# Kernel optimization log

Measured on AMD Instinct MI355X. Metric: run time of the kernel, lower is better.

Reference implementation:

```python
import jax, jax.numpy as jnp
import numpy as np

N_GRAPHS = 256      # graphs in the batch
N_PER = 52          # nodes per peptide graph (module default num_nodes=52)
IN_CH = 21          # amino-acid one-hot features
HIDDEN = 128
OUT_EG = 128
LATENT = 64
N_LAYERS = 4


def _fc_edges(n_graphs, n_per):
    """Block-diagonal fully-connected directed edges (no self loops)."""
    base = np.arange(n_per)
    r, c = np.meshgrid(base, base, indexing='ij')
    mask = r != c
    r, c = r[mask], c[mask]                       # [n_per*(n_per-1)]
    offs = (np.arange(n_graphs) * n_per)[:, None]
    row = (r[None, :] + offs).reshape(-1)
    col = (c[None, :] + offs).reshape(-1)
    return row.astype(np.int32), col.astype(np.int32)


def setup_inputs() -> dict:
    key = jax.random.key(0)
    ks = iter(jax.random.split(key, 40))

    def rn(shape, scale=0.05):
        return jax.random.normal(next(ks), shape, dtype=jnp.float32) * scale

    N = N_GRAPHS * N_PER
    row, col = _fc_edges(N_GRAPHS, N_PER)
    L, H = N_LAYERS, HIDDEN
    return {
        'x': jax.random.normal(next(ks), (N, IN_CH), dtype=jnp.float32),
        'pos': jax.random.normal(next(ks), (N, 3), dtype=jnp.float32),
        'edge_row': jnp.asarray(row),
        'edge_col': jnp.asarray(col),
        'batch': jnp.repeat(jnp.arange(N_GRAPHS, dtype=jnp.int32), N_PER),
        'emb_in_w': rn((IN_CH, H)), 'emb_in_b': jnp.zeros((H,), jnp.float32),
        'edge_w1': rn((L, 2 * H + 1, H)), 'edge_b1': jnp.zeros((L, H), jnp.float32),
        'edge_w2': rn((L, H, H)), 'edge_b2': jnp.zeros((L, H), jnp.float32),
        'node_w1': rn((L, 2 * H, H)), 'node_b1': jnp.zeros((L, H), jnp.float32),
        'node_w2': rn((L, H, H)), 'node_b2': jnp.zeros((L, H), jnp.float32),
        'coord_w1': rn((L, H, H)), 'coord_b1': jnp.zeros((L, H), jnp.float32),
        'coord_w2': rn((L, H, 1), scale=0.001),   # xavier gain=0.001, no bias
        'emb_out_w': rn((H, OUT_EG)), 'emb_out_b': jnp.zeros((OUT_EG,), jnp.float32),
        'mean_w': rn((OUT_EG, LATENT)), 'mean_b': jnp.zeros((LATENT,), jnp.float32),
        'logvar_w': rn((OUT_EG, LATENT)), 'logvar_b': jnp.zeros((LATENT,), jnp.float32),
    }


def _segment_mean(data, ids, n):
    s = jax.ops.segment_sum(data, ids, num_segments=n)
    cnt = jax.ops.segment_sum(jnp.ones((data.shape[0],), data.dtype), ids, num_segments=n)
    return s / jnp.clip(cnt, 1.0)[:, None]


def _egcl(h, coord, row, col, p):
    """One E_GCL layer (residual=True, coords_agg='mean', no attention/tanh/normalize)."""
    ew1, eb1, ew2, eb2, nw1, nb1, nw2, nb2, cw1, cb1, cw2 = p
    n = h.shape[0]
    coord_diff = coord[row] - coord[col]                     # [E,3]
    radial = jnp.sum(coord_diff * coord_diff, axis=1, keepdims=True)  # [E,1]
    # edge model
    m = jnp.concatenate([h[row], h[col], radial], axis=1)    # [E,2H+1]
    m = jax.nn.silu(m @ ew1 + eb1)
    edge_feat = jax.nn.silu(m @ ew2 + eb2)                   # [E,H]
    # coord model: per-edge scalar, mean-aggregated onto source nodes
    t = jax.nn.silu(edge_feat @ cw1 + cb1) @ cw2             # [E,1]
    coord = coord + _segment_mean(coord_diff * t, row, n)
    # node model: sum-aggregate edge features, MLP, residual
    agg = jax.ops.segment_sum(edge_feat, row, num_segments=n)
    z = jnp.concatenate([h, agg], axis=1)                    # [N,2H]
    z = jax.nn.silu(z @ nw1 + nb1)
    h = h + (z @ nw2 + nb2)
    return h, coord


def reference(x, pos, edge_row, edge_col, batch,
              emb_in_w, emb_in_b,
              edge_w1, edge_b1, edge_w2, edge_b2,
              node_w1, node_b1, node_w2, node_b2,
              coord_w1, coord_b1, coord_w2,
              emb_out_w, emb_out_b,
              mean_w, mean_b, logvar_w, logvar_b):
    h = x @ emb_in_w + emb_in_b
    coord = pos
    for i in range(edge_w1.shape[0]):
        h, coord = _egcl(h, coord, edge_row, edge_col,
                         (edge_w1[i], edge_b1[i], edge_w2[i], edge_b2[i],
                          node_w1[i], node_b1[i], node_w2[i], node_b2[i],
                          coord_w1[i], coord_b1[i], coord_w2[i]))
    h = h @ emb_out_w + emb_out_b                            # embedding_out
    g = _segment_mean(h, batch, N_GRAPHS)                    # global_mean_pool
    mean = g @ mean_w + mean_b
    log_var = g @ logvar_w + logvar_b
    return mean, log_var
```

## Files before the change

### kernel.cpp

```cpp
#include <hip/hip_runtime.h>

constexpr int NPER = 52;
constexpr int HID  = 128;
constexpr int INCH = 21;
constexpr int NLAY = 4;
constexpr int LATD = 64;
constexpr int NGRAPH = 256;
constexpr int TPB  = 1024;
constexpr int TSTR = 424;
constexpr int TILE = 16 * TSTR;

typedef short short8 __attribute__((ext_vector_type(8)));
typedef float f32x4  __attribute__((ext_vector_type(4)));

constexpr int W1T_OFF = 0;
constexpr int W1T_SZ  = NLAY * 256 * HID;
constexpr int W2T_OFF = W1T_OFF + W1T_SZ;
constexpr int W2T_SZ  = NLAY * HID * HID;
constexpr int C1T_OFF = W2T_OFF + W2T_SZ;
constexpr int C1T_SZ  = NLAY * HID * HID;
constexpr int N1T_OFF = C1T_OFF + C1T_SZ;
constexpr int N1T_SZ  = NLAY * HID * 2 * HID;
constexpr int N2T_OFF = N1T_OFF + N1T_SZ;
constexpr int N2T_SZ  = NLAY * HID * HID;
constexpr int WS_ELEMS = N2T_OFF + N2T_SZ;

__device__ __forceinline__ unsigned cvt_pk_bf16(float a, float b) {
    unsigned r;
    asm("v_cvt_pk_bf16_f32 %0, %1, %2" : "=v"(r) : "v"(a), "v"(b));
    return r;
}
__device__ __forceinline__ unsigned short f2bf(float f) {
    return (unsigned short)cvt_pk_bf16(f, f);
}
__device__ __forceinline__ float bf2f(unsigned short h) {
    return __uint_as_float(((unsigned)h) << 16);
}
__device__ __forceinline__ float fast_rcp(float x) {
    float r;
    asm("v_rcp_f32 %0, %1" : "=v"(r) : "v"(x));
    return r;
}
__device__ __forceinline__ float silu_f(float v) {
    return v * fast_rcp(1.0f + __expf(-v));
}
__device__ __forceinline__ f32x4 mfma16(short8 a, short8 b, f32x4 c) {
    return __builtin_amdgcn_mfma_f32_16x16x32_bf16(a, b, c, 0, 0, 0);
}

__device__ __forceinline__ int tidx(int row, int e) {
    return (e >> 3) * TSTR + row * 8 + (e & 7);
}

__global__ void conv_w(const float* __restrict__ ew1, const float* __restrict__ ew2,
                       const float* __restrict__ cw1, const float* __restrict__ nw1,
                       const float* __restrict__ nw2, unsigned short* __restrict__ ws)
{
    int idx = blockIdx.x * 256 + threadIdx.x;
    if (idx >= WS_ELEMS) return;
    float v;
    if (idx < W2T_OFF) {
        int t = idx - W1T_OFF;
        int L = t / (256 * HID), rem = t % (256 * HID);
        int n = rem / HID, k = rem % HID;
        v = (n < HID) ? ew1[(size_t)L * 257 * HID + k * HID + n]
                      : ew1[(size_t)L * 257 * HID + (HID + k) * HID + (n - HID)];
    } else if (idx < C1T_OFF) {
        int t = idx - W2T_OFF;
        int L = t / (HID * HID), rem = t % (HID * HID);
        int n = rem / HID, k = rem % HID;
        v = ew2[(size_t)L * HID * HID + k * HID + n];
    } else if (idx < N1T_OFF) {
        int t = idx - C1T_OFF;
        int L = t / (HID * HID), rem = t % (HID * HID);
        int n = rem / HID, k = rem % HID;
        v = cw1[(size_t)L * HID * HID + k * HID + n];
    } else if (idx < N2T_OFF) {
        int t = idx - N1T_OFF;
        int L = t / (HID * 2 * HID), rem = t % (HID * 2 * HID);
        int n = rem / (2 * HID), k = rem % (2 * HID);
        v = nw1[(size_t)L * 2 * HID * HID + k * HID + n];
    } else {
        int t = idx - N2T_OFF;
        int L = t / (HID * HID), rem = t % (HID * HID);
        int n = rem / HID, k = rem % HID;
        v = nw2[(size_t)L * HID * HID + k * HID + n];
    }
    ws[idx] = f2bf(v);
}

constexpr int LDS_FLOATS = 1024 + 156 + 156 + 128 + 512 + 128;
constexpr size_t SHMEM_BYTES = (size_t)8 * TILE * 2 + LDS_FLOATS * 4;

__device__ __forceinline__ void coord_agg(int r, int rr, const float* tpart,
                                          const float* coord_s, float* cacc_s, int lane)
{
    float dx = 0.f, dy = 0.f, dz = 0.f;
    if (lane < NPER) {
        const float* tb = tpart + rr * 256;
        float tc = tb[lane] + tb[64 + lane] + tb[128 + lane] + tb[192 + lane];
        dx = (coord_s[r * 3 + 0] - coord_s[lane * 3 + 0]) * tc;
        dy = (coord_s[r * 3 + 1] - coord_s[lane * 3 + 1]) * tc;
        dz = (coord_s[r * 3 + 2] - coord_s[lane * 3 + 2]) * tc;
    }
    #pragma unroll
    for (int m = 1; m < 64; m <<= 1) {
        dx += __shfl_xor(dx, m); dy += __shfl_xor(dy, m); dz += __shfl_xor(dz, m);
    }
    if (lane == 0) {
        cacc_s[r * 3 + 0] = dx; cacc_s[r * 3 + 1] = dy; cacc_s[r * 3 + 2] = dz;
    }
}

extern "C" __global__ void __launch_bounds__(TPB)
egnn_mfma(const float* __restrict__ x, const float* __restrict__ pos,
          const float* __restrict__ emb_in_w, const float* __restrict__ emb_in_b,
          const float* __restrict__ edge_w1,
          const float* __restrict__ edge_b1, const float* __restrict__ edge_b2,
          const float* __restrict__ node_b1, const float* __restrict__ node_b2,
          const float* __restrict__ coord_b1, const float* __restrict__ coord_w2,
          const float* __restrict__ emb_out_w, const float* __restrict__ emb_out_b,
          const float* __restrict__ mean_w, const float* __restrict__ mean_b,
          const float* __restrict__ logvar_w, const float* __restrict__ logvar_b,
          const unsigned short* __restrict__ ws, float* __restrict__ out)
{
    extern __shared__ __align__(16) char smem[];
    unsigned short* m0_t = (unsigned short*)smem;
    unsigned short* m1_t = m0_t + TILE;
    unsigned short* e0_t = m1_t + TILE;
    unsigned short* e1_t = e0_t + TILE;
    unsigned short* h_t  = e1_t + TILE;
    unsigned short* ag_t = h_t  + TILE;
    unsigned short* A_t  = ag_t + TILE;
    unsigned short* B_t  = A_t  + TILE;
    float* aggp    = (float*)(B_t + TILE);
    float* coord_s = aggp + 1024;
    float* cacc_s  = coord_s + 156;
    float* rad_s   = cacc_s + 156;
    float* tpart   = rad_s + 128;
    float* wr_s    = tpart + 512;

    const int g    = blockIdx.x;
    const int tid  = threadIdx.x;
    const int lane = tid & 63;
    const int wv   = tid >> 6;
    const int mp   = wv >> 2;
    const int np   = wv & 3;
    const int l15  = lane & 15;
    const int kb   = lane >> 4;
    const int rowA = mp * 16 + l15;
    const int crow0 = mp * 16 + kb * 4;
    const int n0   = 32 * np + l15;
    const int n1   = n0 + 16;
    const int jp   = 2 * lane;
    const int pb   = (jp >> 3) * TSTR + (jp & 7);
    const int fo   = kb * TSTR + rowA * 8;

    {
        float* xs = (float*)m0_t;
        for (int p = tid; p < NPER * INCH; p += TPB) xs[p] = x[(size_t)g * NPER * INCH + p];
        for (int p = tid; p < NPER * 3; p += TPB)    coord_s[p] = pos[(size_t)g * NPER * 3 + p];
    }
    __syncthreads();

    for (int p = tid; p < NPER * HID; p += TPB) {
        int c = p >> 7, j = p & 127;
        float s = emb_in_b[j];
        #pragma unroll 7
        for (int k = 0; k < INCH; ++k) s += ((float*)m0_t)[c * INCH + k] * emb_in_w[k * HID + j];
        h_t[tidx(c, j)] = f2bf(s);
    }
    __syncthreads();

    for (int L = 0; L < NLAY; ++L) {
        const unsigned short* w1t = ws + W1T_OFF + (size_t)L * 256 * HID;
        const unsigned short* w2t = ws + W2T_OFF + (size_t)L * HID * HID;
        const unsigned short* c1t = ws + C1T_OFF + (size_t)L * HID * HID;
        const unsigned short* n1t = ws + N1T_OFF + (size_t)L * HID * 2 * HID;
        const unsigned short* n2t = ws + N2T_OFF + (size_t)L * HID * HID;

        short8 wE[8], wC[8];
        #pragma unroll
        for (int s = 0; s < 4; ++s) {
            wE[s]     = *(const short8*)(w2t + (size_t)n0 * HID + 32 * s + 8 * kb);
            wE[4 + s] = *(const short8*)(w2t + (size_t)n1 * HID + 32 * s + 8 * kb);
            wC[s]     = *(const short8*)(c1t + (size_t)n0 * HID + 32 * s + 8 * kb);
            wC[4 + s] = *(const short8*)(c1t + (size_t)n1 * HID + 32 * s + 8 * kb);
        }
        float eb2v[2], cb1v[2], cw2v[2];
        eb2v[0] = edge_b2[L * HID + n0];  eb2v[1] = edge_b2[L * HID + n1];
        cb1v[0] = coord_b1[L * HID + n0]; cb1v[1] = coord_b1[L * HID + n1];
        cw2v[0] = coord_w2[L * HID + n0]; cw2v[1] = coord_w2[L * HID + n1];
        if (tid < HID) wr_s[tid] = edge_w1[(size_t)L * 257 * HID + 256 * HID + tid];

        {
            f32x4 acc[4];
            #pragma unroll
            for (int q = 0; q < 4; ++q) acc[q] = (f32x4){0.f, 0.f, 0.f, 0.f};
            #pragma unroll
            for (int s = 0; s < 4; ++s) {
                short8 af = *(const short8*)(h_t + fo + s * 4 * TSTR);
                #pragma unroll
                for (int q = 0; q < 4; ++q) {
                    int n = l15 + 16 * (4 * np + q);
                    short8 bf = *(const short8*)(w1t + (size_t)n * HID + 32 * s + 8 * kb);
                    acc[q] = mfma16(af, bf, acc[q]);
                }
            }
            #pragma unroll
            for (int q = 0; q < 4; ++q) {
                int n = l15 + 16 * (4 * np + q);
                float eb1 = (n < HID) ? edge_b1[L * HID + n] : 0.f;
                #pragma unroll
                for (int reg = 0; reg < 4; ++reg) {
                    int c = crow0 + reg;
                    if (c < NPER) {
                        float v = acc[q][reg] + eb1;
                        if (n < HID) A_t[tidx(c, n)] = f2bf(v);
                        else         B_t[tidx(c, n - HID)] = f2bf(v);
                    }
                }
            }
        }
        if (tid < NPER) {
            float dx = coord_s[0] - coord_s[tid * 3 + 0];
            float dy = coord_s[1] - coord_s[tid * 3 + 1];
            float dz = coord_s[2] - coord_s[tid * 3 + 2];
            rad_s[tid] = dx * dx + dy * dy + dz * dz;
        } else if (tid >= 64 && tid < 64 + NPER) {
            int c = tid - 64;
            float dx = coord_s[3] - coord_s[c * 3 + 0];
            float dy = coord_s[4] - coord_s[c * 3 + 1];
            float dz = coord_s[5] - coord_s[c * 3 + 2];
            rad_s[64 + c] = dx * dx + dy * dy + dz * dz;
        }
        __syncthreads();

        const float wrl = wr_s[jp], wrh = wr_s[jp + 1];

        for (int gp = 0; gp < 26; ++gp) {
            const int r0 = 2 * gp, r1 = r0 + 1;

            {
                unsigned pa0 = *(const unsigned*)(A_t + pb + r0 * 8);
                unsigned pa1 = *(const unsigned*)(A_t + pb + r1 * 8);
                float A0l = bf2f((unsigned short)(pa0 & 0xffff)), A0h = bf2f((unsigned short)(pa0 >> 16));
                float A1l = bf2f((unsigned short)(pa1 & 0xffff)), A1h = bf2f((unsigned short)(pa1 >> 16));
                for (int j = wv; j < 2 * NPER; j += 16) {
                    int rr = (j >= NPER);
                    int c  = rr ? j - NPER : j;
                    float Al = rr ? A1l : A0l, Ah = rr ? A1h : A0h;
                    float rad = rad_s[rr * 64 + c];
                    unsigned bp = *(const unsigned*)(B_t + pb + c * 8);
                    float v0 = Al + bf2f((unsigned short)(bp & 0xffff)) + rad * wrl;
                    float v1 = Ah + bf2f((unsigned short)(bp >> 16))    + rad * wrh;
                    unsigned mv = cvt_pk_bf16(silu_f(v0), silu_f(v1));
                    *(unsigned*)((rr ? m1_t : m0_t) + pb + c * 8) = mv;
                }
            }
            __syncthreads();

            {
                f32x4 e00 = (f32x4){0.f,0.f,0.f,0.f}, e01 = e00, e10 = e00, e11 = e00;
                #pragma unroll
                for (int s = 0; s < 4; ++s) {
                    short8 af0 = *(const short8*)(m0_t + fo + s * 4 * TSTR);
                    short8 af1 = *(const short8*)(m1_t + fo + s * 4 * TSTR);
                    e00 = mfma16(af0, wE[s], e00); e01 = mfma16(af0, wE[4 + s], e01);
                    e10 = mfma16(af1, wE[s], e10); e11 = mfma16(af1, wE[4 + s], e11);
                }
                #pragma unroll
                for (int rr = 0; rr < 2; ++rr) {
                    f32x4 ea = rr ? e10 : e00, eb = rr ? e11 : e01;
                    unsigned short* et = rr ? e1_t : e0_t;
                    const int r = rr ? r1 : r0;
                    float a0 = 0.f, a1 = 0.f;
                    #pragma unroll
                    for (int reg = 0; reg < 4; ++reg) {
                        int c = crow0 + reg;
                        float v0 = silu_f(ea[reg] + eb2v[0]);
                        float v1 = silu_f(eb[reg] + eb2v[1]);
                        if (c < NPER) {
                            et[tidx(c, n0)] = f2bf(v0);
                            et[tidx(c, n1)] = f2bf(v1);
                            if (c != r) { a0 += v0; a1 += v1; }
                        }
                    }
                    a0 += __shfl_xor(a0, 16); a0 += __shfl_xor(a0, 32);
                    a1 += __shfl_xor(a1, 16); a1 += __shfl_xor(a1, 32);
                    if (kb == 0) {
                        float* ar = aggp + (rr * 4 + mp) * HID;
                        ar[n0] = a0; ar[n1] = a1;
                    }
                }
                if (wv < 2 && gp > 0) coord_agg(2 * gp - 2 + wv, wv, tpart, coord_s, cacc_s, lane);
            }
            __syncthreads();

            {
                f32x4 y00 = (f32x4){0.f,0.f,0.f,0.f}, y01 = y00, y10 = y00, y11 = y00;
                #pragma unroll
                for (int s = 0; s < 4; ++s) {
                    short8 af0 = *(const short8*)(e0_t + fo + s * 4 * TSTR);
                    short8 af1 = *(const short8*)(e1_t + fo + s * 4 * TSTR);
                    y00 = mfma16(af0, wC[s], y00); y01 = mfma16(af0, wC[4 + s], y01);
                    y10 = mfma16(af1, wC[s], y10); y11 = mfma16(af1, wC[4 + s], y11);
                }
                #pragma unroll
                for (int rr = 0; rr < 2; ++rr) {
                    f32x4 ya = rr ? y10 : y00, yb = rr ? y11 : y01;
                    float* tp = tpart + (rr * 4 + np) * 64;
                    #pragma unroll
                    for (int reg = 0; reg < 4; ++reg) {
                        float v = silu_f(ya[reg] + cb1v[0]) * cw2v[0]
                                + silu_f(yb[reg] + cb1v[1]) * cw2v[1];
                        v += __shfl_xor(v, 1); v += __shfl_xor(v, 2);
                        v += __shfl_xor(v, 4); v += __shfl_xor(v, 8);
                        if (l15 == 0) tp[crow0 + reg] = v;
                    }
                }
            }
            if (tid < 256) {
                int rr = tid >> 7, t = tid & 127;
                const float* ap = aggp + rr * 512;
                float a = ap[t] + ap[128 + t] + ap[256 + t] + ap[384 + t];
                ag_t[tidx(2 * gp + rr, t)] = f2bf(a);
            } else if (tid < 384 && gp + 1 < 26) {
                int t = tid - 256, rr = t >> 6, c = t & 63;
                if (c < NPER) {
                    int r = 2 * (gp + 1) + rr;
                    float dx = coord_s[r * 3 + 0] - coord_s[c * 3 + 0];
                    float dy = coord_s[r * 3 + 1] - coord_s[c * 3 + 1];
                    float dz = coord_s[r * 3 + 2] - coord_s[c * 3 + 2];
                    rad_s[rr * 64 + c] = dx * dx + dy * dy + dz * dz;
                }
            }
            __syncthreads();
        }

        if (wv < 2) coord_agg(50 + wv, wv, tpart, coord_s, cacc_s, lane);
        {
            float nb1v[2];
            nb1v[0] = node_b1[L * HID + n0]; nb1v[1] = node_b1[L * HID + n1];
            f32x4 z0 = (f32x4){0.f,0.f,0.f,0.f}, z1 = z0;
            #pragma unroll
            for (int s = 0; s < 4; ++s) {
                short8 af = *(const short8*)(h_t + fo + s * 4 * TSTR);
                z0 = mfma16(af, *(const short8*)(n1t + (size_t)n0 * 2 * HID + 32 * s + 8 * kb), z0);
                z1 = mfma16(af, *(const short8*)(n1t + (size_t)n1 * 2 * HID + 32 * s + 8 * kb), z1);
            }
            #pragma unroll
            for (int s = 0; s < 4; ++s) {
                short8 af = *(const short8*)(ag_t + fo + s * 4 * TSTR);
                z0 = mfma16(af, *(const short8*)(n1t + (size_t)n0 * 2 * HID + HID + 32 * s + 8 * kb), z0);
                z1 = mfma16(af, *(const short8*)(n1t + (size_t)n1 * 2 * HID + HID + 32 * s + 8 * kb), z1);
            }
            #pragma unroll
            for (int reg = 0; reg < 4; ++reg) {
                int c = crow0 + reg;
                if (c < NPER) {
                    m0_t[tidx(c, n0)] = f2bf(silu_f(z0[reg] + nb1v[0]));
                    m0_t[tidx(c, n1)] = f2bf(silu_f(z1[reg] + nb1v[1]));
                }
            }
        }
        __syncthreads();

        if (tid < NPER * 3) coord_s[tid] += cacc_s[tid] * (1.0f / 51.0f);
        {
            float nb2v[2];
            nb2v[0] = node_b2[L * HID + n0]; nb2v[1] = node_b2[L * HID + n1];
            f32x4 d0 = (f32x4){0.f,0.f,0.f,0.f}, d1 = d0;
            #pragma unroll
            for (int s = 0; s < 4; ++s) {
                short8 af = *(const short8*)(m0_t + fo + s * 4 * TSTR);
                d0 = mfma16(af, *(const short8*)(n2t + (size_t)n0 * HID + 32 * s + 8 * kb), d0);
                d1 = mfma16(af, *(const short8*)(n2t + (size_t)n1 * HID + 32 * s + 8 * kb), d1);
            }
            #pragma unroll
            for (int reg = 0; reg < 4; ++reg) {
                int c = crow0 + reg;
                if (c < NPER) {
                    int i0 = tidx(c, n0), i1 = tidx(c, n1);
                    h_t[i0] = f2bf(bf2f(h_t[i0]) + d0[reg] + nb2v[0]);
                    h_t[i1] = f2bf(bf2f(h_t[i1]) + d1[reg] + nb2v[1]);
                }
            }
        }
        __syncthreads();
    }

    float* gm = aggp;
    float* eg = aggp + HID;
    if (tid < HID) {
        float s = 0.f;
        for (int c = 0; c < NPER; ++c) s += bf2f(h_t[tidx(c, tid)]);
        gm[tid] = s * (1.0f / 52.0f);
    }
    __syncthreads();
    if (tid < HID) {
        float s = emb_out_b[tid];
        #pragma unroll 4
        for (int k = 0; k < HID; ++k) s += gm[k] * emb_out_w[k * HID + tid];
        eg[tid] = s;
    }
    __syncthreads();
    if (tid < 2 * LATD) {
        const int  l   = tid & (LATD - 1);
        const bool ism = tid < LATD;
        const float* W = ism ? mean_w : logvar_w;
        float s = ism ? mean_b[l] : logvar_b[l];
        #pragma unroll 4
        for (int k = 0; k < HID; ++k) s += eg[k] * W[k * LATD + l];
        out[(ism ? 0 : NGRAPH * LATD) + g * LATD + l] = s;
    }
}

extern "C" void kernel_launch(void* const* d_in, const int* in_sizes, int n_in,
                              void* d_out, int out_size, void* d_ws, size_t ws_size,
                              hipStream_t stream) {
    const float* x         = (const float*)d_in[0];
    const float* pos       = (const float*)d_in[1];
    const float* emb_in_w  = (const float*)d_in[5];
    const float* emb_in_b  = (const float*)d_in[6];
    const float* edge_w1   = (const float*)d_in[7];
    const float* edge_b1   = (const float*)d_in[8];
    const float* edge_w2   = (const float*)d_in[9];
    const float* edge_b2   = (const float*)d_in[10];
    const float* node_w1   = (const float*)d_in[11];
    const float* node_b1   = (const float*)d_in[12];
    const float* node_w2   = (const float*)d_in[13];
    const float* node_b2   = (const float*)d_in[14];
    const float* coord_w1  = (const float*)d_in[15];
    const float* coord_b1  = (const float*)d_in[16];
    const float* coord_w2  = (const float*)d_in[17];
    const float* emb_out_w = (const float*)d_in[18];
    const float* emb_out_b = (const float*)d_in[19];
    const float* mean_w    = (const float*)d_in[20];
    const float* mean_b    = (const float*)d_in[21];
    const float* logvar_w  = (const float*)d_in[22];
    const float* logvar_b  = (const float*)d_in[23];

    unsigned short* ws = (unsigned short*)d_ws;

    conv_w<<<(WS_ELEMS + 255) / 256, 256, 0, stream>>>(edge_w1, edge_w2, coord_w1,
                                                       node_w1, node_w2, ws);

    (void)hipFuncSetAttribute(reinterpret_cast<const void*>(egnn_mfma),
                              hipFuncAttributeMaxDynamicSharedMemorySize,
                              (int)SHMEM_BYTES);

    hipLaunchKernelGGL(egnn_mfma, dim3(NGRAPH), dim3(TPB), SHMEM_BYTES, stream,
                       x, pos, emb_in_w, emb_in_b, edge_w1,
                       edge_b1, edge_b2, node_b1, node_b2,
                       coord_b1, coord_w2, emb_out_w, emb_out_b,
                       mean_w, mean_b, logvar_w, logvar_b,
                       ws, (float*)d_out);
}
```

Measured before the change: 805.7 us.

## Software-pipeline per-row edge stages into one barrier per phase

Replaces the two-rows-per-iteration loop, which had three barriers per row pair, with a 54-phase software pipeline. Each phase runs the edge-MLP MFMA for row r, the coord-MLP MFMA for row r-1, the message SiLU for row r+1, plus the aggregate reduction, radial and coordinate-update work on dedicated waves, all behind a single barrier. Weight fragments are now read from global/L2 inside the loop instead of being held in registers. The message step is vectorised to 4 elements per thread with the B operand hoisted, and SiLU uses raw exp/rcp instructions. This aims to cut barrier count and idle time, at the cost of repeated weight reloads and more pipeline logic.

```diff
diff --git a/kernel.cpp b/kernel.cpp
--- a/kernel.cpp
+++ b/kernel.cpp
@@ -1,11 +1,6 @@
 #include <hip/hip_runtime.h>
 
-constexpr int NPER = 52;
-constexpr int HID  = 128;
-constexpr int INCH = 21;
-constexpr int NLAY = 4;
-constexpr int LATD = 64;
-constexpr int NGRAPH = 256;
+constexpr int NPER = 52, HID = 128, INCH = 21, NLAY = 4, LATD = 64, NGRAPH = 256;
 constexpr int TPB  = 1024;
 constexpr int TSTR = 424;
 constexpr int TILE = 16 * TSTR;
@@ -13,16 +8,11 @@
 typedef short short8 __attribute__((ext_vector_type(8)));
 typedef float f32x4  __attribute__((ext_vector_type(4)));
 
-constexpr int W1T_OFF = 0;
-constexpr int W1T_SZ  = NLAY * 256 * HID;
-constexpr int W2T_OFF = W1T_OFF + W1T_SZ;
-constexpr int W2T_SZ  = NLAY * HID * HID;
-constexpr int C1T_OFF = W2T_OFF + W2T_SZ;
-constexpr int C1T_SZ  = NLAY * HID * HID;
-constexpr int N1T_OFF = C1T_OFF + C1T_SZ;
-constexpr int N1T_SZ  = NLAY * HID * 2 * HID;
-constexpr int N2T_OFF = N1T_OFF + N1T_SZ;
-constexpr int N2T_SZ  = NLAY * HID * HID;
+constexpr int W1T_OFF = 0,                 W1T_SZ = NLAY * 256 * HID;
+constexpr int W2T_OFF = W1T_OFF + W1T_SZ,  W2T_SZ = NLAY * HID * HID;
+constexpr int C1T_OFF = W2T_OFF + W2T_SZ,  C1T_SZ = NLAY * HID * HID;
+constexpr int N1T_OFF = C1T_OFF + C1T_SZ,  N1T_SZ = NLAY * HID * 2 * HID;
+constexpr int N2T_OFF = N1T_OFF + N1T_SZ,  N2T_SZ = NLAY * HID * HID;
 constexpr int WS_ELEMS = N2T_OFF + N2T_SZ;
 
 __device__ __forceinline__ unsigned cvt_pk_bf16(float a, float b) {
@@ -36,18 +26,17 @@
 __device__ __forceinline__ float bf2f(unsigned short h) {
     return __uint_as_float(((unsigned)h) << 16);
 }
-__device__ __forceinline__ float fast_rcp(float x) {
-    float r;
-    asm("v_rcp_f32 %0, %1" : "=v"(r) : "v"(x));
-    return r;
-}
+__device__ __forceinline__ float blo(unsigned u) { return __uint_as_float(u << 16); }
+__device__ __forceinline__ float bhi(unsigned u) { return __uint_as_float(u & 0xffff0000u); }
 __device__ __forceinline__ float silu_f(float v) {
-    return v * fast_rcp(1.0f + __expf(-v));
+    float e, r;
+    asm("v_exp_f32 %0, %1" : "=v"(e) : "v"(v * -1.44269504088896341f));
+    asm("v_rcp_f32 %0, %1" : "=v"(r) : "v"(1.0f + e));
+    return v * r;
 }
 __device__ __forceinline__ f32x4 mfma16(short8 a, short8 b, f32x4 c) {
     return __builtin_amdgcn_mfma_f32_16x16x32_bf16(a, b, c, 0, 0, 0);
 }
-
 __device__ __forceinline__ int tidx(int row, int e) {
     return (e >> 3) * TSTR + row * 8 + (e & 7);
 }
@@ -89,28 +78,8 @@
     ws[idx] = f2bf(v);
 }
 
-constexpr int LDS_FLOATS = 1024 + 156 + 156 + 128 + 512 + 128;
+constexpr int LDS_FLOATS = 1024 + 512 + 128 + 156 + 156 + 128;
 constexpr size_t SHMEM_BYTES = (size_t)8 * TILE * 2 + LDS_FLOATS * 4;
-
-__device__ __forceinline__ void coord_agg(int r, int rr, const float* tpart,
-                                          const float* coord_s, float* cacc_s, int lane)
-{
-    float dx = 0.f, dy = 0.f, dz = 0.f;
-    if (lane < NPER) {
-        const float* tb = tpart + rr * 256;
-        float tc = tb[lane] + tb[64 + lane] + tb[128 + lane] + tb[192 + lane];
-        dx = (coord_s[r * 3 + 0] - coord_s[lane * 3 + 0]) * tc;
-        dy = (coord_s[r * 3 + 1] - coord_s[lane * 3 + 1]) * tc;
-        dz = (coord_s[r * 3 + 2] - coord_s[lane * 3 + 2]) * tc;
-    }
-    #pragma unroll
-    for (int m = 1; m < 64; m <<= 1) {
-        dx += __shfl_xor(dx, m); dy += __shfl_xor(dy, m); dz += __shfl_xor(dz, m);
-    }
-    if (lane == 0) {
-        cacc_s[r * 3 + 0] = dx; cacc_s[r * 3 + 1] = dy; cacc_s[r * 3 + 2] = dz;
-    }
-}
 
 extern "C" __global__ void __launch_bounds__(TPB)
 egnn_mfma(const float* __restrict__ x, const float* __restrict__ pos,
@@ -134,11 +103,11 @@
     unsigned short* A_t  = ag_t + TILE;
     unsigned short* B_t  = A_t  + TILE;
     float* aggp    = (float*)(B_t + TILE);
-    float* coord_s = aggp + 1024;
+    float* tpart   = aggp + 1024;
+    float* rad_s   = tpart + 512;
+    float* coord_s = rad_s + 128;
     float* cacc_s  = coord_s + 156;
-    float* rad_s   = cacc_s + 156;
-    float* tpart   = rad_s + 128;
-    float* wr_s    = tpart + 512;
+    float* wr_s    = cacc_s + 156;
 
     const int g    = blockIdx.x;
     const int tid  = threadIdx.x;
@@ -152,9 +121,13 @@
     const int crow0 = mp * 16 + kb * 4;
     const int n0   = 32 * np + l15;
     const int n1   = n0 + 16;
-    const int jp   = 2 * lane;
-    const int pb   = (jp >> 3) * TSTR + (jp & 7);
+    const int ebA  = (n0 >> 3) * TSTR + (n0 & 7);
+    const int ebB  = (n1 >> 3) * TSTR + (n1 & 7);
     const int fo   = kb * TSTR + rowA * 8;
+    const int mrow0 = tid >> 5;
+    const int mrow1 = mrow0 + 32;
+    const int c4    = (tid & 31) * 4;
+    const int pb4   = (c4 >> 3) * TSTR + (c4 & 7);
 
     {
         float* xs = (float*)m0_t;
@@ -179,18 +152,9 @@
         const unsigned short* n1t = ws + N1T_OFF + (size_t)L * HID * 2 * HID;
         const unsigned short* n2t = ws + N2T_OFF + (size_t)L * HID * HID;
 
-        short8 wE[8], wC[8];
-        #pragma unroll
-        for (int s = 0; s < 4; ++s) {
-            wE[s]     = *(const short8*)(w2t + (size_t)n0 * HID + 32 * s + 8 * kb);
-            wE[4 + s] = *(const short8*)(w2t + (size_t)n1 * HID + 32 * s + 8 * kb);
-            wC[s]     = *(const short8*)(c1t + (size_t)n0 * HID + 32 * s + 8 * kb);
-            wC[4 + s] = *(const short8*)(c1t + (size_t)n1 * HID + 32 * s + 8 * kb);
-        }
-        float eb2v[2], cb1v[2], cw2v[2];
-        eb2v[0] = edge_b2[L * HID + n0];  eb2v[1] = edge_b2[L * HID + n1];
-        cb1v[0] = coord_b1[L * HID + n0]; cb1v[1] = coord_b1[L * HID + n1];
-        cw2v[0] = coord_w2[L * HID + n0]; cw2v[1] = coord_w2[L * HID + n1];
+        const float eb2v0 = edge_b2[L * HID + n0],  eb2v1 = edge_b2[L * HID + n1];
+        const float cb1v0 = coord_b1[L * HID + n0], cb1v1 = coord_b1[L * HID + n1];
+        const float cw2v0 = coord_w2[L * HID + n0], cw2v1 = coord_w2[L * HID + n1];
         if (tid < HID) wr_s[tid] = edge_w1[(size_t)L * 257 * HID + 256 * HID + tid];
 
         {
@@ -221,128 +185,149 @@
                     }
                 }
             }
-        }
-        if (tid < NPER) {
-            float dx = coord_s[0] - coord_s[tid * 3 + 0];
-            float dy = coord_s[1] - coord_s[tid * 3 + 1];
-            float dz = coord_s[2] - coord_s[tid * 3 + 2];
-            rad_s[tid] = dx * dx + dy * dy + dz * dz;
-        } else if (tid >= 64 && tid < 64 + NPER) {
-            int c = tid - 64;
-            float dx = coord_s[3] - coord_s[c * 3 + 0];
-            float dy = coord_s[4] - coord_s[c * 3 + 1];
-            float dz = coord_s[5] - coord_s[c * 3 + 2];
-            rad_s[64 + c] = dx * dx + dy * dy + dz * dz;
+            if ((wv == 14 || wv == 15) && lane < NPER) {
+                int r = wv - 14;
+                float dx = coord_s[r * 3 + 0] - coord_s[lane * 3 + 0];
+                float dy = coord_s[r * 3 + 1] - coord_s[lane * 3 + 1];
+                float dz = coord_s[r * 3 + 2] - coord_s[lane * 3 + 2];
+                rad_s[(r & 1) * 64 + lane] = dx * dx + dy * dy + dz * dz;
+            }
         }
         __syncthreads();
 
-        const float wrl = wr_s[jp], wrh = wr_s[jp + 1];
-
-        for (int gp = 0; gp < 26; ++gp) {
-            const int r0 = 2 * gp, r1 = r0 + 1;
-
+        float w4x, w4y, w4z, w4w;
+        { float4 t4 = *(const float4*)(wr_s + c4); w4x = t4.x; w4y = t4.y; w4z = t4.z; w4w = t4.w; }
+        float Bf0[4] = {0.f, 0.f, 0.f, 0.f}, Bf1[4] = {0.f, 0.f, 0.f, 0.f};
+        {
+            uint2 b = *(const uint2*)(B_t + pb4 + mrow0 * 8);
+            Bf0[0] = blo(b.x); Bf0[1] = bhi(b.x); Bf0[2] = blo(b.y); Bf0[3] = bhi(b.y);
+        }
+        if (mrow1 < NPER) {
+            uint2 b = *(const uint2*)(B_t + pb4 + mrow1 * 8);
+            Bf1[0] = blo(b.x); Bf1[1] = bhi(b.x); Bf1[2] = blo(b.y); Bf1[3] = bhi(b.y);
+        }
+
+        auto mstep = [&](int rn) {
+            unsigned short* mt = (rn & 1) ? m1_t : m0_t;
+            uint2 a = *(const uint2*)(A_t + pb4 + rn * 8);
+            float A0 = blo(a.x), A1 = bhi(a.x), A2 = blo(a.y), A3 = bhi(a.y);
+            const float* radp = rad_s + (rn & 1) * 64;
             {
-                unsigned pa0 = *(const unsigned*)(A_t + pb + r0 * 8);
-                unsigned pa1 = *(const unsigned*)(A_t + pb + r1 * 8);
-                float A0l = bf2f((unsigned short)(pa0 & 0xffff)), A0h = bf2f((unsigned short)(pa0 >> 16));
-                float A1l = bf2f((unsigned short)(pa1 & 0xffff)), A1h = bf2f((unsigned short)(pa1 >> 16));
-                for (int j = wv; j < 2 * NPER; j += 16) {
-                    int rr = (j >= NPER);
-                    int c  = rr ? j - NPER : j;
-                    float Al = rr ? A1l : A0l, Ah = rr ? A1h : A0h;
-                    float rad = rad_s[rr * 64 + c];
-                    unsigned bp = *(const unsigned*)(B_t + pb + c * 8);
-                    float v0 = Al + bf2f((unsigned short)(bp & 0xffff)) + rad * wrl;
-                    float v1 = Ah + bf2f((unsigned short)(bp >> 16))    + rad * wrh;
-                    unsigned mv = cvt_pk_bf16(silu_f(v0), silu_f(v1));
-                    *(unsigned*)((rr ? m1_t : m0_t) + pb + c * 8) = mv;
+                float rad = radp[mrow0];
+                uint2 o;
+                o.x = cvt_pk_bf16(silu_f(A0 + Bf0[0] + rad * w4x), silu_f(A1 + Bf0[1] + rad * w4y));
+                o.y = cvt_pk_bf16(silu_f(A2 + Bf0[2] + rad * w4z), silu_f(A3 + Bf0[3] + rad * w4w));
+                *(uint2*)(mt + pb4 + mrow0 * 8) = o;
+            }
+            if (mrow1 < NPER) {
+                float rad = radp[mrow1];
+                uint2 o;
+                o.x = cvt_pk_bf16(silu_f(A0 + Bf1[0] + rad * w4x), silu_f(A1 + Bf1[1] + rad * w4y));
+                o.y = cvt_pk_bf16(silu_f(A2 + Bf1[2] + rad * w4z), silu_f(A3 + Bf1[3] + rad * w4w));
+                *(uint2*)(mt + pb4 + mrow1 * 8) = o;
+            }
+        };
+
+        mstep(0);
+        __syncthreads();
+
+        for (int ph = 0; ph < 54; ++ph) {
+            if (ph < 52) {
+                const int r = ph;
+                const unsigned short* mcur = (r & 1) ? m1_t : m0_t;
+                unsigned short* ecur = (r & 1) ? e1_t : e0_t;
+                f32x4 ea = (f32x4){0.f, 0.f, 0.f, 0.f}, eb = ea;
+                #pragma unroll
+                for (int s = 0; s < 4; ++s) {
+                    short8 af = *(const short8*)(mcur + fo + s * 4 * TSTR);
+                    ea = mfma16(af, *(const short8*)(w2t + (size_t)n0 * HID + 32 * s + 8 * kb), ea);
+                    eb = mfma16(af, *(const short8*)(w2t + (size_t)n1 * HID + 32 * s + 8 * kb), eb);
+                }
+                float a0 = 0.f, a1 = 0.f;
+                #pragma unroll
+                for (int reg = 0; reg < 4; ++reg) {
+                    int c = crow0 + reg;
+                    float v0 = silu_f(ea[reg] + eb2v0);
+                    float v1 = silu_f(eb[reg] + eb2v1);
+                    if (c < NPER) {
+                        ecur[ebA + c * 8] = f2bf(v0);
+                        ecur[ebB + c * 8] = f2bf(v1);
+                        if (c != r) { a0 += v0; a1 += v1; }
+                    }
+                }
+                a0 += __shfl_xor(a0, 16); a0 += __shfl_xor(a0, 32);
+                a1 += __shfl_xor(a1, 16); a1 += __shfl_xor(a1, 32);
+                if (kb == 0) {
+                    float* ar = aggp + (r & 1) * 512 + mp * HID;
+                    ar[n0] = a0; ar[n1] = a1;
+                }
+            }
+
+            if (ph >= 1 && ph <= 52) {
+                const int rp = ph - 1;
+                const unsigned short* ecur = (rp & 1) ? e1_t : e0_t;
+                f32x4 ya = (f32x4){0.f, 0.f, 0.f, 0.f}, yb = ya;
+                #pragma unroll
+                for (int s = 0; s < 4; ++s) {
+                    short8 af = *(const short8*)(ecur + fo + s * 4 * TSTR);
+                    ya = mfma16(af, *(const short8*)(c1t + (size_t)n0 * HID + 32 * s + 8 * kb), ya);
+                    yb = mfma16(af, *(const short8*)(c1t + (size_t)n1 * HID + 32 * s + 8 * kb), yb);
+                }
+                float* tp = tpart + (rp & 1) * 256 + np * 64;
+                #pragma unroll
+                for (int reg = 0; reg < 4; ++reg) {
+                    float v = silu_f(ya[reg] + cb1v0) * cw2v0 + silu_f(yb[reg] + cb1v1) * cw2v1;
+                    v += __shfl_xor(v, 1); v += __shfl_xor(v, 2);
+                    v += __shfl_xor(v, 4); v += __shfl_xor(v, 8);
+                    if (l15 == 0) tp[crow0 + reg] = v;
+                }
+            }
+
+            if (ph + 1 < 52) mstep(ph + 1);
+
+            if (wv == 12 || wv == 13) {
+                if (ph >= 1 && ph <= 52) {
+                    const int rf = ph - 1;
+                    int t = (wv - 12) * 64 + lane;
+                    const float* ap = aggp + (rf & 1) * 512;
+                    float a = ap[t] + ap[128 + t] + ap[256 + t] + ap[384 + t];
+                    ag_t[(t >> 3) * TSTR + rf * 8 + (t & 7)] = f2bf(a);
+                }
+            } else if (wv == 14) {
+                if (ph + 2 < 52 && lane < NPER) {
+                    const int rn = ph + 2;
+                    float dx = coord_s[rn * 3 + 0] - coord_s[lane * 3 + 0];
+                    float dy = coord_s[rn * 3 + 1] - coord_s[lane * 3 + 1];
+                    float dz = coord_s[rn * 3 + 2] - coord_s[lane * 3 + 2];
+                    rad_s[(rn & 1) * 64 + lane] = dx * dx + dy * dy + dz * dz;
+                }
+            } else if (wv == 15) {
+                if (ph >= 2) {
+                    const int rc = ph - 2;
+                    const float* tb = tpart + (rc & 1) * 256;
+                    float dx = 0.f, dy = 0.f, dz = 0.f;
+                    if (lane < NPER) {
+                        float tc = tb[lane] + tb[64 + lane] + tb[128 + lane] + tb[192 + lane];
+                        dx = (coord_s[rc * 3 + 0] - coord_s[lane * 3 + 0]) * tc;
+                        dy = (coord_s[rc * 3 + 1] - coord_s[lane * 3 + 1]) * tc;
+                        dz = (coord_s[rc * 3 + 2] - coord_s[lane * 3 + 2]) * tc;
+                    }
+                    #pragma unroll
+                    for (int m = 1; m < 64; m <<= 1) {
+                        dx += __shfl_xor(dx, m); dy += __shfl_xor(dy, m); dz += __shfl_xor(dz, m);
+                    }
+                    if (lane == 0) {
+                        cacc_s[rc * 3 + 0] = dx; cacc_s[rc * 3 + 1] = dy; cacc_s[rc * 3 + 2] = dz;
+                    }
                 }
             }
             __syncthreads();
-
-            {
-                f32x4 e00 = (f32x4){0.f,0.f,0.f,0.f}, e01 = e00, e10 = e00, e11 = e00;
-                #pragma unroll
-                for (int s = 0; s < 4; ++s) {
-                    short8 af0 = *(const short8*)(m0_t + fo + s * 4 * TSTR);
-                    short8 af1 = *(const short8*)(m1_t + fo + s * 4 * TSTR);
-                    e00 = mfma16(af0, wE[s], e00); e01 = mfma16(af0, wE[4 + s], e01);
-                    e10 = mfma16(af1, wE[s], e10); e11 = mfma16(af1, wE[4 + s], e11);
-                }
-                #pragma unroll
-                for (int rr = 0; rr < 2; ++rr) {
-                    f32x4 ea = rr ? e10 : e00, eb = rr ? e11 : e01;
-                    unsigned short* et = rr ? e1_t : e0_t;
-                    const int r = rr ? r1 : r0;
-                    float a0 = 0.f, a1 = 0.f;
-                    #pragma unroll
-                    for (int reg = 0; reg < 4; ++reg) {
-                        int c = crow0 + reg;
-                        float v0 = silu_f(ea[reg] + eb2v[0]);
-                        float v1 = silu_f(eb[reg] + eb2v[1]);
-                        if (c < NPER) {
-                            et[tidx(c, n0)] = f2bf(v0);
-                            et[tidx(c, n1)] = f2bf(v1);
-                            if (c != r) { a0 += v0; a1 += v1; }
-                        }
-                    }
-                    a0 += __shfl_xor(a0, 16); a0 += __shfl_xor(a0, 32);
-                    a1 += __shfl_xor(a1, 16); a1 += __shfl_xor(a1, 32);
-                    if (kb == 0) {
-                        float* ar = aggp + (rr * 4 + mp) * HID;
-                        ar[n0] = a0; ar[n1] = a1;
-                    }
-                }
-                if (wv < 2 && gp > 0) coord_agg(2 * gp - 2 + wv, wv, tpart, coord_s, cacc_s, lane);
-            }
-            __syncthreads();
-
-            {
-                f32x4 y00 = (f32x4){0.f,0.f,0.f,0.f}, y01 = y00, y10 = y00, y11 = y00;
-                #pragma unroll
-                for (int s = 0; s < 4; ++s) {
-                    short8 af0 = *(const short8*)(e0_t + fo + s * 4 * TSTR);
-                    short8 af1 = *(const short8*)(e1_t + fo + s * 4 * TSTR);
-                    y00 = mfma16(af0, wC[s], y00); y01 = mfma16(af0, wC[4 + s], y01);
-                    y10 = mfma16(af1, wC[s], y10); y11 = mfma16(af1, wC[4 + s], y11);
-                }
-                #pragma unroll
-                for (int rr = 0; rr < 2; ++rr) {
-                    f32x4 ya = rr ? y10 : y00, yb = rr ? y11 : y01;
-                    float* tp = tpart + (rr * 4 + np) * 64;
-                    #pragma unroll
-                    for (int reg = 0; reg < 4; ++reg) {
-                        float v = silu_f(ya[reg] + cb1v[0]) * cw2v[0]
-                                + silu_f(yb[reg] + cb1v[1]) * cw2v[1];
-                        v += __shfl_xor(v, 1); v += __shfl_xor(v, 2);
-                        v += __shfl_xor(v, 4); v += __shfl_xor(v, 8);
-                        if (l15 == 0) tp[crow0 + reg] = v;
-                    }
-                }
-            }
-            if (tid < 256) {
-                int rr = tid >> 7, t = tid & 127;
-                const float* ap = aggp + rr * 512;
-                float a = ap[t] + ap[128 + t] + ap[256 + t] + ap[384 + t];
-                ag_t[tidx(2 * gp + rr, t)] = f2bf(a);
-            } else if (tid < 384 && gp + 1 < 26) {
-                int t = tid - 256, rr = t >> 6, c = t & 63;
-                if (c < NPER) {
-                    int r = 2 * (gp + 1) + rr;
-                    float dx = coord_s[r * 3 + 0] - coord_s[c * 3 + 0];
-                    float dy = coord_s[r * 3 + 1] - coord_s[c * 3 + 1];
-                    float dz = coord_s[r * 3 + 2] - coord_s[c * 3 + 2];
-                    rad_s[rr * 64 + c] = dx * dx + dy * dy + dz * dz;
-                }
-            }
-            __syncthreads();
-        }
-
-        if (wv < 2) coord_agg(50 + wv, wv, tpart, coord_s, cacc_s, lane);
+        }
+
+        if (tid < NPER * 3) coord_s[tid] += cacc_s[tid] * (1.0f / 51.0f);
         {
-            float nb1v[2];
-            nb1v[0] = node_b1[L * HID + n0]; nb1v[1] = node_b1[L * HID + n1];
-            f32x4 z0 = (f32x4){0.f,0.f,0.f,0.f}, z1 = z0;
+            const float nb1v0 = node_b1[L * HID + n0], nb1v1 = node_b1[L * HID + n1];
+            f32x4 z0 = (f32x4){0.f, 0.f, 0.f, 0.f}, z1 = z0;
             #pragma unroll
             for (int s = 0; s < 4; ++s) {
                 short8 af = *(const short8*)(h_t + fo + s * 4 * TSTR);
@@ -359,18 +344,16 @@
             for (int reg = 0; reg < 4; ++reg) {
                 int c = crow0 + reg;
                 if (c < NPER) {
-                    m0_t[tidx(c, n0)] = f2bf(silu_f(z0[reg] + nb1v[0]));
-                    m0_t[tidx(c, n1)] = f2bf(silu_f(z1[reg] + nb1v[1]));
+                    m0_t[tidx(c, n0)] = f2bf(silu_f(z0[reg] + nb1v0));
+                    m0_t[tidx(c, n1)] = f2bf(silu_f(z1[reg] + nb1v1));
                 }
             }
         }
         __syncthreads();
 
-        if (tid < NPER * 3) coord_s[tid] += cacc_s[tid] * (1.0f / 51.0f);
         {
-            float nb2v[2];
-            nb2v[0] = node_b2[L * HID + n0]; nb2v[1] = node_b2[L * HID + n1];
-            f32x4 d0 = (f32x4){0.f,0.f,0.f,0.f}, d1 = d0;
+            const float nb2v0 = node_b2[L * HID + n0], nb2v1 = node_b2[L * HID + n1];
+            f32x4 d0 = (f32x4){0.f, 0.f, 0.f, 0.f}, d1 = d0;
             #pragma unroll
             for (int s = 0; s < 4; ++s) {
                 short8 af = *(const short8*)(m0_t + fo + s * 4 * TSTR);
@@ -382,8 +365,8 @@
                 int c = crow0 + reg;
                 if (c < NPER) {
                     int i0 = tidx(c, n0), i1 = tidx(c, n1);
-                    h_t[i0] = f2bf(bf2f(h_t[i0]) + d0[reg] + nb2v[0]);
-                    h_t[i1] = f2bf(bf2f(h_t[i1]) + d1[reg] + nb2v[1]);
+                    h_t[i0] = f2bf(bf2f(h_t[i0]) + d0[reg] + nb2v0);
+                    h_t[i1] = f2bf(bf2f(h_t[i1]) + d1[reg] + nb2v1);
                 }
             }
         }
@@ -441,10 +424,10 @@
     const float* logvar_w  = (const float*)d_in[22];
     const float* logvar_b  = (const float*)d_in[23];
 
-    unsigned short* ws = (unsigned short*)d_ws;
+    unsigned short* wsu = (unsigned short*)d_ws;
 
     conv_w<<<(WS_ELEMS + 255) / 256, 256, 0, stream>>>(edge_w1, edge_w2, coord_w1,
-                                                       node_w1, node_w2, ws);
+                                                       node_w1, node_w2, wsu);
 
     (void)hipFuncSetAttribute(reinterpret_cast<const void*>(egnn_mfma),
                               hipFuncAttributeMaxDynamicSharedMemorySize,
@@ -455,5 +438,5 @@
                        edge_b1, edge_b2, node_b1, node_b2,
                        coord_b1, coord_w2, emb_out_w, emb_out_b,
                        mean_w, mean_b, logvar_w, logvar_b,
-                       ws, (float*)d_out);
-}
+                       wsu, (float*)d_out);
+}
```

Result: slower. 1.956 ms (+142.8%).
